# Optimization experiments

Hardware: AMD Instinct MI355X
Metric: run time of the kernel (lower is better)

## Reference

```python
import jax, jax.numpy as jnp
import numpy as np

N = 50000      # nodes per type
E = 600000     # edges per relation
D_IN = 128
D_OUT = 64


def setup_inputs() -> dict:
    key = jax.random.key(0)
    ks = jax.random.split(key, 12)
    x_v0 = jax.random.normal(ks[0], (N, D_IN), dtype=jnp.float32)
    x_v1 = jax.random.normal(ks[1], (N, D_IN), dtype=jnp.float32)
    edge_v0 = jax.random.randint(ks[2], (2, E), 0, N, dtype=jnp.int64)
    edge_v1 = jax.random.randint(ks[3], (2, E), 0, N, dtype=jnp.int64)
    s = 1.0 / np.sqrt(D_IN)
    Wrel0 = jax.random.uniform(ks[4], (D_OUT, D_IN), jnp.float32, -s, s)
    brel0 = jax.random.uniform(ks[5], (D_OUT,), jnp.float32, -s, s)
    Wroot0 = jax.random.uniform(ks[6], (D_OUT, D_IN), jnp.float32, -s, s)
    Wrel1 = jax.random.uniform(ks[7], (D_OUT, D_IN), jnp.float32, -s, s)
    brel1 = jax.random.uniform(ks[8], (D_OUT,), jnp.float32, -s, s)
    Wroot1 = jax.random.uniform(ks[9], (D_OUT, D_IN), jnp.float32, -s, s)
    sf = 1.0 / np.sqrt(2 * D_OUT)
    Wfc = jax.random.uniform(ks[10], (1, 2 * D_OUT), jnp.float32, -sf, sf)
    bfc = jax.random.uniform(ks[11], (1,), jnp.float32, -sf, sf)
    return {"x_v0": x_v0, "x_v1": x_v1, "edge_v0": edge_v0, "edge_v1": edge_v1,
            "Wrel0": Wrel0, "brel0": brel0, "Wroot0": Wroot0,
            "Wrel1": Wrel1, "brel1": brel1, "Wroot1": Wroot1,
            "Wfc": Wfc, "bfc": bfc}


def _graph_conv(x, edge_index, Wrel, brel, Wroot):
    # PyG GraphConv (aggr='add'): out = lin_rel(sum_{j in N(i)} x_j) + lin_root(x_i)
    src, dst = edge_index[0], edge_index[1]
    agg = jax.ops.segment_sum(x[src], dst, num_segments=x.shape[0])  # [N, D_IN]
    return agg @ Wrel.T + brel + x @ Wroot.T


def reference(x_v0, x_v1, edge_v0, edge_v1, Wrel0, brel0, Wroot0,
              Wrel1, brel1, Wroot1, Wfc, bfc):
    h0 = jax.nn.relu(_graph_conv(x_v0, edge_v0, Wrel0, brel0, Wroot0))  # [N, 64]
    h1 = jax.nn.relu(_graph_conv(x_v1, edge_v1, Wrel1, brel1, Wroot1))  # [N, 64]
    h = jnp.concatenate([h0, h1], axis=1)  # [N, 128]
    return h @ Wfc.T + bfc  # [N, 1]
```

## Files before the change

### kernel.cpp

```cpp
#include <hip/hip_runtime.h>
#include <hip/hip_bf16.h>

typedef __attribute__((ext_vector_type(8))) short short8;
typedef __attribute__((ext_vector_type(4))) float floatx4;

#define NB    1000
#define BPN   50
#define BCAP  832
#define CHUNK 2048

static __device__ __forceinline__ unsigned short bf16_of(float f) {
    union { float f; unsigned u; } v; v.f = f;
    unsigned r = (v.u + 0x7FFF + ((v.u >> 16) & 1)) >> 16;
    return (unsigned short)r;
}
static __device__ __forceinline__ float lo_f(unsigned u) {
    union { float f; unsigned u; } v; v.u = u << 16; return v.f;
}
static __device__ __forceinline__ float hi_f(unsigned u) {
    union { float f; unsigned u; } v; v.u = u & 0xFFFF0000u; return v.f;
}

__global__ __launch_bounds__(256) void convert_w(
    const float* __restrict__ Wrel0, const float* __restrict__ Wroot0,
    const float* __restrict__ Wrel1, const float* __restrict__ Wroot1,
    unsigned short* __restrict__ Wb0, unsigned short* __restrict__ Wb1)
{
    int c = blockIdx.x * 256 + threadIdx.x;
    if (c >= 4096) return;
    const float* s; unsigned short* d;
    if      (c < 1024) { s = Wrel0 + c * 8;           d = Wb0 + c * 8; }
    else if (c < 2048) { int t = c - 1024; s = Wroot0 + t * 8; d = Wb0 + 8192 + t * 8; }
    else if (c < 3072) { int t = c - 2048; s = Wrel1 + t * 8;  d = Wb1 + t * 8; }
    else               { int t = c - 3072; s = Wroot1 + t * 8; d = Wb1 + 8192 + t * 8; }

    floatx4 v0 = *(const floatx4*)s;
    floatx4 v1 = *(const floatx4*)(s + 4);
    short8 r = { (short)bf16_of(v0[0]), (short)bf16_of(v0[1]),
                 (short)bf16_of(v0[2]), (short)bf16_of(v0[3]),
                 (short)bf16_of(v1[0]), (short)bf16_of(v1[1]),
                 (short)bf16_of(v1[2]), (short)bf16_of(v1[3]) };
    *(short8*)d = r;
}

__global__ __launch_bounds__(256) void gemm_mfma(
    const float* __restrict__ X0, const float* __restrict__ X1,
    const unsigned short* __restrict__ Wb0, const unsigned short* __restrict__ Wb1,
    unsigned short* __restrict__ Yrel0, unsigned short* __restrict__ Yrel1,
    unsigned short* __restrict__ Yroot0, unsigned short* __restrict__ Yroot1,
    int N)
{
    const float* X           = blockIdx.y ? X1 : X0;
    const unsigned short* Wb = blockIdx.y ? Wb1 : Wb0;
    unsigned short* Yrel     = blockIdx.y ? Yrel1 : Yrel0;
    unsigned short* Yroot    = blockIdx.y ? Yroot1 : Yroot0;

    __shared__ __align__(16) short x_sh[128 * 136];
    __shared__ __align__(16) short w_sh[128 * 136];

    const int tid = threadIdx.x;
    const int m0  = blockIdx.x * 128;

#pragma unroll
    for (int i = 0; i < 8; ++i) {
        int c   = tid + 256 * i;
        int row = c >> 4;
        int kc  = (c & 15) * 8;
        *(short8*)&w_sh[row * 136 + kc] = *(const short8*)(Wb + row * 128 + kc);
    }
#pragma unroll
    for (int i = 0; i < 16; ++i) {
        int c    = tid + 256 * i;
        int row  = c >> 5;
        int f    = (c & 31) * 4;
        int node = m0 + row;
        floatx4 v = {};
        if (node < N) v = *(const floatx4*)(X + (size_t)node * 128 + f);
        short* d = &x_sh[row * 136 + f];
        d[0] = (short)bf16_of(v[0]); d[1] = (short)bf16_of(v[1]);
        d[2] = (short)bf16_of(v[2]); d[3] = (short)bf16_of(v[3]);
    }
    __syncthreads();

    const int wv   = tid >> 6;
    const int lane = tid & 63;
    const int q    = lane >> 4;
    const int r    = lane & 15;

    floatx4 acc[2][8] = {};
#pragma unroll
    for (int ko = 0; ko < 4; ++ko) {
        int kb = ko * 32 + q * 8;
        short8 a0 = *(const short8*)&x_sh[(wv * 32 + r) * 136 + kb];
        short8 a1 = *(const short8*)&x_sh[(wv * 32 + 16 + r) * 136 + kb];
#pragma unroll
        for (int nt = 0; nt < 8; ++nt) {
            short8 b = *(const short8*)&w_sh[(nt * 16 + r) * 136 + kb];
            acc[0][nt] = __builtin_amdgcn_mfma_f32_16x16x32_bf16(a0, b, acc[0][nt], 0, 0, 0);
            acc[1][nt] = __builtin_amdgcn_mfma_f32_16x16x32_bf16(a1, b, acc[1][nt], 0, 0, 0);
        }
    }

#pragma unroll
    for (int mt = 0; mt < 2; ++mt)
#pragma unroll
        for (int nt = 0; nt < 8; ++nt) {
            int col = nt * 16 + r;
#pragma unroll
            for (int reg = 0; reg < 4; ++reg) {
                int row = m0 + wv * 32 + mt * 16 + q * 4 + reg;
                if (row < N) {
                    if (nt < 4) Yrel[(size_t)row * 64 + col] = bf16_of(acc[mt][nt][reg]);
                    else        Yroot[(size_t)row * 64 + (col - 64)] = bf16_of(acc[mt][nt][reg]);
                }
            }
        }
}

__global__ __launch_bounds__(256) void bucket_pass(
    const int* __restrict__ e0, const int* __restrict__ e1,
    unsigned int* __restrict__ pairs0, unsigned int* __restrict__ pairs1,
    int* __restrict__ cur0, int* __restrict__ cur1, int E, int N)
{
    const int* e        = blockIdx.y ? e1 : e0;
    unsigned int* pairs = blockIdx.y ? pairs1 : pairs0;
    int* cur            = blockIdx.y ? cur1 : cur0;

    __shared__ unsigned int   stage[CHUNK];
    __shared__ unsigned short sbuck[CHUNK];
    __shared__ int hist[NB];
    __shared__ int loff[NB];
    __shared__ int lcur[NB];
    __shared__ int gbase[NB];
    __shared__ int scanb[256];

    const int tid = threadIdx.x;
    const int c0  = blockIdx.x * CHUNK;
    const int n   = min(CHUNK, E - c0);

    for (int b = tid; b < NB; b += 256) hist[b] = 0;
    __syncthreads();

#pragma unroll
    for (int k = 0; k < CHUNK / 256; ++k) {
        int i = c0 + k * 256 + tid;
        if (i < c0 + n) {
            int dst = e[E + i];
            if ((unsigned)dst < (unsigned)N)
                atomicAdd(&hist[(unsigned)dst / BPN], 1);
        }
    }
    __syncthreads();

    int t4 = tid * 4, v[4], s = 0;
#pragma unroll
    for (int k = 0; k < 4; ++k) {
        int b = t4 + k;
        v[k] = (b < NB) ? hist[b] : 0;
        s += v[k];
    }
    scanb[tid] = s;
    __syncthreads();
    for (int off = 1; off < 256; off <<= 1) {
        int x = (tid >= off) ? scanb[tid - off] : 0;
        __syncthreads();
        scanb[tid] += x;
        __syncthreads();
    }
    int run = scanb[tid] - s;
#pragma unroll
    for (int k = 0; k < 4; ++k) {
        int b = t4 + k;
        if (b < NB) { loff[b] = run; lcur[b] = run; }
        run += v[k];
    }
    for (int b = tid; b < NB; b += 256)
        gbase[b] = (hist[b] > 0) ? atomicAdd(&cur[b], hist[b]) : 0;
    __syncthreads();

#pragma unroll
    for (int k = 0; k < CHUNK / 256; ++k) {
        int i = c0 + k * 256 + tid;
        if (i < c0 + n) {
            int src = e[i];
            int dst = e[E + i];
            if ((unsigned)dst < (unsigned)N) {
                unsigned usrc = ((unsigned)src < (unsigned)N) ? (unsigned)src : 0u;
                int b = (unsigned)dst / BPN;
                int p = atomicAdd(&lcur[b], 1);
                stage[p] = ((unsigned)dst << 16) | usrc;
                sbuck[p] = (unsigned short)b;
            }
        }
    }
    __syncthreads();

    int total = scanb[255];
    for (int p = tid; p < total; p += 256) {
        int b = sbuck[p];
        int g = gbase[b] + (p - loff[b]);
        if (g < BCAP)
            pairs[(size_t)b * BCAP + g] = stage[p];
    }
}

__global__ __launch_bounds__(512) void bucket_gather(
    const unsigned int* __restrict__ pairs0, const unsigned int* __restrict__ pairs1,
    const int* __restrict__ cur0, const int* __restrict__ cur1,
    const unsigned short* __restrict__ Yrel0, const unsigned short* __restrict__ Yrel1,
    const unsigned short* __restrict__ Yroot0, const unsigned short* __restrict__ Yroot1,
    const float* __restrict__ brel0, const float* __restrict__ brel1,
    const float* __restrict__ wfc, const float* __restrict__ bfc,
    float* __restrict__ out, int N)
{
    __shared__ unsigned short slist0[BCAP], slist1[BCAP];
    __shared__ int cnt0s[BPN], cnt1s[BPN];
    __shared__ int off0s[BPN], off1s[BPN];
    __shared__ int cur0s[BPN], cur1s[BPN];

    const int tid  = threadIdx.x;
    const int b    = blockIdx.x;
    const int wv   = tid >> 6;
    const int lane = tid & 63;
    const int c    = lane & 31;
    const int half = lane >> 5;

    for (int i = tid; i < BPN; i += 512) { cnt0s[i] = 0; cnt1s[i] = 0; }
    __syncthreads();

    const int n0 = min(cur0[b], BCAP);
    const int n1 = min(cur1[b], BCAP);
    const unsigned base = (unsigned)(b * BPN);

    for (int j = tid; j < n0; j += 512)
        atomicAdd(&cnt0s[(pairs0[(size_t)b * BCAP + j] >> 16) - base], 1);
    for (int j = tid; j < n1; j += 512)
        atomicAdd(&cnt1s[(pairs1[(size_t)b * BCAP + j] >> 16) - base], 1);
    __syncthreads();

    if (wv == 0) {
        int cc = (lane < BPN) ? cnt0s[lane] : 0;
        int inc = cc;
#pragma unroll
        for (int d = 1; d < 64; d <<= 1) {
            int t = __shfl_up(inc, d, 64);
            if (lane >= d) inc += t;
        }
        if (lane < BPN) { off0s[lane] = inc - cc; cur0s[lane] = inc - cc; }
    } else if (wv == 1) {
        int cc = (lane < BPN) ? cnt1s[lane] : 0;
        int inc = cc;
#pragma unroll
        for (int d = 1; d < 64; d <<= 1) {
            int t = __shfl_up(inc, d, 64);
            if (lane >= d) inc += t;
        }
        if (lane < BPN) { off1s[lane] = inc - cc; cur1s[lane] = inc - cc; }
    }
    __syncthreads();

    for (int j = tid; j < n0; j += 512) {
        unsigned p = pairs0[(size_t)b * BCAP + j];
        int pos = atomicAdd(&cur0s[(p >> 16) - base], 1);
        slist0[pos] = (unsigned short)(p & 0xFFFFu);
    }
    for (int j = tid; j < n1; j += 512) {
        unsigned p = pairs1[(size_t)b * BCAP + j];
        int pos = atomicAdd(&cur1s[(p >> 16) - base], 1);
        slist1[pos] = (unsigned short)(p & 0xFFFFu);
    }
    __syncthreads();

    const float2 br0 = ((const float2*)brel0)[c];
    const float2 br1 = ((const float2*)brel1)[c];
    const float2 w0  = ((const float2*)wfc)[c];
    const float2 w1  = ((const float2*)(wfc + 64))[c];
    const float bias = bfc[0];

    for (int nl = wv; nl < BPN; nl += 8) {
        int i = b * BPN + nl;
        float a0x = 0.f, a0y = 0.f, a1x = 0.f, a1y = 0.f;

        {
            int st = off0s[nl], d = cnt0s[nl], j = 0;
            for (; j + 7 < d; j += 8) {
                int i0 = slist0[st + j + half];
                int i1 = slist0[st + j + 2 + half];
                int i2 = slist0[st + j + 4 + half];
                int i3 = slist0[st + j + 6 + half];
                unsigned u0 = ((const unsigned*)(Yrel0 + ((size_t)i0 << 6)))[c];
                unsigned u1 = ((const unsigned*)(Yrel0 + ((size_t)i1 << 6)))[c];
                unsigned u2 = ((const unsigned*)(Yrel0 + ((size_t)i2 << 6)))[c];
                unsigned u3 = ((const unsigned*)(Yrel0 + ((size_t)i3 << 6)))[c];
                a0x += (lo_f(u0) + lo_f(u1)) + (lo_f(u2) + lo_f(u3));
                a0y += (hi_f(u0) + hi_f(u1)) + (hi_f(u2) + hi_f(u3));
            }
            for (; j < d; j += 2) {
                int jj = j + half;
                int idx = slist0[st + (jj < d ? jj : d - 1)];
                unsigned u = ((const unsigned*)(Yrel0 + ((size_t)idx << 6)))[c];
                if (jj < d) { a0x += lo_f(u); a0y += hi_f(u); }
            }
        }
        {
            int st = off1s[nl], d = cnt1s[nl], j = 0;
            for (; j + 7 < d; j += 8) {
                int i0 = slist1[st + j + half];
                int i1 = slist1[st + j + 2 + half];
                int i2 = slist1[st + j + 4 + half];
                int i3 = slist1[st + j + 6 + half];
                unsigned u0 = ((const unsigned*)(Yrel1 + ((size_t)i0 << 6)))[c];
                unsigned u1 = ((const unsigned*)(Yrel1 + ((size_t)i1 << 6)))[c];
                unsigned u2 = ((const unsigned*)(Yrel1 + ((size_t)i2 << 6)))[c];
                unsigned u3 = ((const unsigned*)(Yrel1 + ((size_t)i3 << 6)))[c];
                a1x += (lo_f(u0) + lo_f(u1)) + (lo_f(u2) + lo_f(u3));
                a1y += (hi_f(u0) + hi_f(u1)) + (hi_f(u2) + hi_f(u3));
            }
            for (; j < d; j += 2) {
                int jj = j + half;
                int idx = slist1[st + (jj < d ? jj : d - 1)];
                unsigned u = ((const unsigned*)(Yrel1 + ((size_t)idx << 6)))[c];
                if (jj < d) { a1x += lo_f(u); a1y += hi_f(u); }
            }
        }

        a0x += __shfl_xor(a0x, 32, 64);
        a0y += __shfl_xor(a0y, 32, 64);
        a1x += __shfl_xor(a1x, 32, 64);
        a1y += __shfl_xor(a1y, 32, 64);

        unsigned ur0 = ((const unsigned*)(Yroot0 + ((size_t)i << 6)))[c];
        unsigned ur1 = ((const unsigned*)(Yroot1 + ((size_t)i << 6)))[c];

        float h0x = fmaxf(a0x + br0.x + lo_f(ur0), 0.f);
        float h0y = fmaxf(a0y + br0.y + hi_f(ur0), 0.f);
        float h1x = fmaxf(a1x + br1.x + lo_f(ur1), 0.f);
        float h1y = fmaxf(a1y + br1.y + hi_f(ur1), 0.f);
        float s = h0x * w0.x + h0y * w0.y + h1x * w1.x + h1y * w1.y;

#pragma unroll
        for (int m = 16; m > 0; m >>= 1) s += __shfl_xor(s, m, 64);
        if (lane == 0) out[i] = s + bias;
    }
}

extern "C" void kernel_launch(void* const* d_in, const int* in_sizes, int n_in,
                              void* d_out, int out_size, void* d_ws, size_t ws_size,
                              hipStream_t stream)
{
    const int N = in_sizes[0] / 128;
    const int E = in_sizes[2] / 2;

    const float* x0     = (const float*)d_in[0];
    const float* x1     = (const float*)d_in[1];
    const int*   e0     = (const int*)d_in[2];
    const int*   e1     = (const int*)d_in[3];
    const float* Wrel0  = (const float*)d_in[4];
    const float* brel0  = (const float*)d_in[5];
    const float* Wroot0 = (const float*)d_in[6];
    const float* Wrel1  = (const float*)d_in[7];
    const float* brel1  = (const float*)d_in[8];
    const float* Wroot1 = (const float*)d_in[9];
    const float* wfc    = (const float*)d_in[10];
    const float* bfc    = (const float*)d_in[11];
    float* out = (float*)d_out;

    unsigned short* Wb0   = (unsigned short*)d_ws;
    unsigned short* Wb1   = Wb0 + 128 * 128;
    unsigned short* Yrel0 = Wb1 + 128 * 128;
    unsigned short* Yrel1 = Yrel0 + (size_t)N * 64;
    unsigned short* Yroot0 = Yrel1 + (size_t)N * 64;
    unsigned short* Yroot1 = Yroot0 + (size_t)N * 64;
    unsigned int* pairs0 = (unsigned int*)(Yroot1 + (size_t)N * 64);
    unsigned int* pairs1 = pairs0 + (size_t)NB * BCAP;
    int* cur0 = (int*)(pairs1 + (size_t)NB * BCAP);
    int* cur1 = cur0 + NB;

    (void)hipMemsetAsync(cur0, 0, 2 * NB * sizeof(int), stream);

    convert_w<<<16, 256, 0, stream>>>(Wrel0, Wroot0, Wrel1, Wroot1, Wb0, Wb1);

    dim3 gemm_grid((N + 127) / 128, 2);
    gemm_mfma<<<gemm_grid, 256, 0, stream>>>(x0, x1, Wb0, Wb1,
                                             Yrel0, Yrel1, Yroot0, Yroot1, N);

    dim3 bp_grid((E + CHUNK - 1) / CHUNK, 2);
    bucket_pass<<<bp_grid, 256, 0, stream>>>(e0, e1, pairs0, pairs1,
                                             cur0, cur1, E, N);

    bucket_gather<<<NB, 512, 0, stream>>>(pairs0, pairs1, cur0, cur1,
                                          Yrel0, Yrel1, Yroot0, Yroot1,
                                          brel0, brel1, wfc, bfc, out, N);
}
```

Baseline: 193.1 us.

## Fuse GEMM and edge bucketing into one launch, fold memset into weight conversion

```diff
diff --git a/kernel.cpp b/kernel.cpp
--- a/kernel.cpp
+++ b/kernel.cpp
@@ -8,6 +8,7 @@
 #define BPN   50
 #define BCAP  832
 #define CHUNK 2048
+#define NPASS 293
 
 static __device__ __forceinline__ unsigned short bf16_of(float f) {
     union { float f; unsigned u; } v; v.f = f;
@@ -24,10 +25,14 @@
 __global__ __launch_bounds__(256) void convert_w(
     const float* __restrict__ Wrel0, const float* __restrict__ Wroot0,
     const float* __restrict__ Wrel1, const float* __restrict__ Wroot1,
-    unsigned short* __restrict__ Wb0, unsigned short* __restrict__ Wb1)
+    unsigned short* __restrict__ Wb0, unsigned short* __restrict__ Wb1,
+    int* __restrict__ cur0, int* __restrict__ cur1)
 {
     int c = blockIdx.x * 256 + threadIdx.x;
+    if (c < NB)          cur0[c] = 0;
+    else if (c < 2 * NB) cur1[c - NB] = 0;
     if (c >= 4096) return;
+
     const float* s; unsigned short* d;
     if      (c < 1024) { s = Wrel0 + c * 8;           d = Wb0 + c * 8; }
     else if (c < 2048) { int t = c - 1024; s = Wroot0 + t * 8; d = Wb0 + 8192 + t * 8; }
@@ -43,165 +48,163 @@
     *(short8*)d = r;
 }
 
-__global__ __launch_bounds__(256) void gemm_mfma(
+union SmemU {
+    struct { short x_sh[32 * 136]; short w_sh[128 * 136]; } g;
+    struct {
+        unsigned int   stage[CHUNK];
+        unsigned short sbuck[CHUNK];
+        int hist[NB]; int loff[NB]; int lcur[NB]; int gbase[NB];
+        int scanb[256];
+    } p;
+};
+
+__global__ __launch_bounds__(256) void gemm_and_pass(
     const float* __restrict__ X0, const float* __restrict__ X1,
     const unsigned short* __restrict__ Wb0, const unsigned short* __restrict__ Wb1,
     unsigned short* __restrict__ Yrel0, unsigned short* __restrict__ Yrel1,
     unsigned short* __restrict__ Yroot0, unsigned short* __restrict__ Yroot1,
-    int N)
+    const int* __restrict__ e0, const int* __restrict__ e1,
+    unsigned int* __restrict__ pairs0, unsigned int* __restrict__ pairs1,
+    int* __restrict__ cur0, int* __restrict__ cur1, int E, int N)
 {
-    const float* X           = blockIdx.y ? X1 : X0;
-    const unsigned short* Wb = blockIdx.y ? Wb1 : Wb0;
-    unsigned short* Yrel     = blockIdx.y ? Yrel1 : Yrel0;
-    unsigned short* Yroot    = blockIdx.y ? Yroot1 : Yroot0;
-
-    __shared__ __align__(16) short x_sh[128 * 136];
-    __shared__ __align__(16) short w_sh[128 * 136];
-
+    __shared__ __align__(16) SmemU sm;
     const int tid = threadIdx.x;
-    const int m0  = blockIdx.x * 128;
+    const int rel = blockIdx.y;
+
+    if (blockIdx.x < NPASS) {
+        const int* e        = rel ? e1 : e0;
+        unsigned int* pairs = rel ? pairs1 : pairs0;
+        int* cur            = rel ? cur1 : cur0;
+
+        const int c0 = blockIdx.x * CHUNK;
+        const int n  = min(CHUNK, E - c0);
+
+        for (int b = tid; b < NB; b += 256) sm.p.hist[b] = 0;
+        __syncthreads();
+
+        int dsts[CHUNK / 256];
+#pragma unroll
+        for (int k = 0; k < CHUNK / 256; ++k) {
+            int i = c0 + k * 256 + tid;
+            int dst = (i < c0 + n) ? e[E + i] : -1;
+            dsts[k] = dst;
+            if ((unsigned)dst < (unsigned)N)
+                atomicAdd(&sm.p.hist[(unsigned)dst / BPN], 1);
+        }
+        __syncthreads();
+
+        int t4 = tid * 4, v[4], s = 0;
+#pragma unroll
+        for (int k = 0; k < 4; ++k) {
+            int b = t4 + k;
+            v[k] = (b < NB) ? sm.p.hist[b] : 0;
+            s += v[k];
+        }
+        sm.p.scanb[tid] = s;
+        __syncthreads();
+        for (int off = 1; off < 256; off <<= 1) {
+            int x = (tid >= off) ? sm.p.scanb[tid - off] : 0;
+            __syncthreads();
+            sm.p.scanb[tid] += x;
+            __syncthreads();
+        }
+        int run = sm.p.scanb[tid] - s;
+#pragma unroll
+        for (int k = 0; k < 4; ++k) {
+            int b = t4 + k;
+            if (b < NB) { sm.p.loff[b] = run; sm.p.lcur[b] = run; }
+            run += v[k];
+        }
+        for (int b = tid; b < NB; b += 256)
+            sm.p.gbase[b] = (sm.p.hist[b] > 0) ? atomicAdd(&cur[b], sm.p.hist[b]) : 0;
+        __syncthreads();
+
+#pragma unroll
+        for (int k = 0; k < CHUNK / 256; ++k) {
+            int i   = c0 + k * 256 + tid;
+            int dst = dsts[k];
+            if ((unsigned)dst < (unsigned)N) {
+                int src = e[i];
+                unsigned usrc = ((unsigned)src < (unsigned)N) ? (unsigned)src : 0u;
+                int b = (unsigned)dst / BPN;
+                int p = atomicAdd(&sm.p.lcur[b], 1);
+                sm.p.stage[p] = ((unsigned)dst << 16) | usrc;
+                sm.p.sbuck[p] = (unsigned short)b;
+            }
+        }
+        __syncthreads();
+
+        int total = sm.p.scanb[255];
+        for (int p = tid; p < total; p += 256) {
+            int b = sm.p.sbuck[p];
+            int g = sm.p.gbase[b] + (p - sm.p.loff[b]);
+            if (g < BCAP)
+                pairs[(size_t)b * BCAP + g] = sm.p.stage[p];
+        }
+        return;
+    }
+
+    const float* X           = rel ? X1 : X0;
+    const unsigned short* Wb = rel ? Wb1 : Wb0;
+    unsigned short* Yrel     = rel ? Yrel1 : Yrel0;
+    unsigned short* Yroot    = rel ? Yroot1 : Yroot0;
+
+    const int m0 = (blockIdx.x - NPASS) * 32;
 
 #pragma unroll
     for (int i = 0; i < 8; ++i) {
         int c   = tid + 256 * i;
         int row = c >> 4;
         int kc  = (c & 15) * 8;
-        *(short8*)&w_sh[row * 136 + kc] = *(const short8*)(Wb + row * 128 + kc);
-    }
-#pragma unroll
-    for (int i = 0; i < 16; ++i) {
+        *(short8*)&sm.g.w_sh[row * 136 + kc] = *(const short8*)(Wb + row * 128 + kc);
+    }
+#pragma unroll
+    for (int i = 0; i < 4; ++i) {
         int c    = tid + 256 * i;
         int row  = c >> 5;
         int f    = (c & 31) * 4;
         int node = m0 + row;
         floatx4 v = {};
         if (node < N) v = *(const floatx4*)(X + (size_t)node * 128 + f);
-        short* d = &x_sh[row * 136 + f];
+        short* d = &sm.g.x_sh[row * 136 + f];
         d[0] = (short)bf16_of(v[0]); d[1] = (short)bf16_of(v[1]);
         d[2] = (short)bf16_of(v[2]); d[3] = (short)bf16_of(v[3]);
     }
     __syncthreads();
 
-    const int wv   = tid >> 6;
+    const int w    = tid >> 6;
     const int lane = tid & 63;
     const int q    = lane >> 4;
     const int r    = lane & 15;
 
-    floatx4 acc[2][8] = {};
+    floatx4 acc[2][2] = {};
 #pragma unroll
     for (int ko = 0; ko < 4; ++ko) {
         int kb = ko * 32 + q * 8;
-        short8 a0 = *(const short8*)&x_sh[(wv * 32 + r) * 136 + kb];
-        short8 a1 = *(const short8*)&x_sh[(wv * 32 + 16 + r) * 136 + kb];
-#pragma unroll
-        for (int nt = 0; nt < 8; ++nt) {
-            short8 b = *(const short8*)&w_sh[(nt * 16 + r) * 136 + kb];
-            acc[0][nt] = __builtin_amdgcn_mfma_f32_16x16x32_bf16(a0, b, acc[0][nt], 0, 0, 0);
-            acc[1][nt] = __builtin_amdgcn_mfma_f32_16x16x32_bf16(a1, b, acc[1][nt], 0, 0, 0);
-        }
+        short8 a0 = *(const short8*)&sm.g.x_sh[(r) * 136 + kb];
+        short8 a1 = *(const short8*)&sm.g.x_sh[(16 + r) * 136 + kb];
+        short8 b0 = *(const short8*)&sm.g.w_sh[(w * 32 + r) * 136 + kb];
+        short8 b1 = *(const short8*)&sm.g.w_sh[(w * 32 + 16 + r) * 136 + kb];
+        acc[0][0] = __builtin_amdgcn_mfma_f32_16x16x32_bf16(a0, b0, acc[0][0], 0, 0, 0);
+        acc[0][1] = __builtin_amdgcn_mfma_f32_16x16x32_bf16(a0, b1, acc[0][1], 0, 0, 0);
+        acc[1][0] = __builtin_amdgcn_mfma_f32_16x16x32_bf16(a1, b0, acc[1][0], 0, 0, 0);
+        acc[1][1] = __builtin_amdgcn_mfma_f32_16x16x32_bf16(a1, b1, acc[1][1], 0, 0, 0);
     }
 
 #pragma unroll
     for (int mt = 0; mt < 2; ++mt)
 #pragma unroll
-        for (int nt = 0; nt < 8; ++nt) {
-            int col = nt * 16 + r;
+        for (int nt = 0; nt < 2; ++nt) {
+            int col = w * 32 + nt * 16 + r;
 #pragma unroll
             for (int reg = 0; reg < 4; ++reg) {
-                int row = m0 + wv * 32 + mt * 16 + q * 4 + reg;
-                if (row < N) {
-                    if (nt < 4) Yrel[(size_t)row * 64 + col] = bf16_of(acc[mt][nt][reg]);
-                    else        Yroot[(size_t)row * 64 + (col - 64)] = bf16_of(acc[mt][nt][reg]);
+                int node = m0 + mt * 16 + q * 4 + reg;
+                if (node < N) {
+                    if (col < 64) Yrel[(size_t)node * 64 + col] = bf16_of(acc[mt][nt][reg]);
+                    else          Yroot[(size_t)node * 64 + (col - 64)] = bf16_of(acc[mt][nt][reg]);
                 }
             }
         }
-}
-
-__global__ __launch_bounds__(256) void bucket_pass(
-    const int* __restrict__ e0, const int* __restrict__ e1,
-    unsigned int* __restrict__ pairs0, unsigned int* __restrict__ pairs1,
-    int* __restrict__ cur0, int* __restrict__ cur1, int E, int N)
-{
-    const int* e        = blockIdx.y ? e1 : e0;
-    unsigned int* pairs = blockIdx.y ? pairs1 : pairs0;
-    int* cur            = blockIdx.y ? cur1 : cur0;
-
-    __shared__ unsigned int   stage[CHUNK];
-    __shared__ unsigned short sbuck[CHUNK];
-    __shared__ int hist[NB];
-    __shared__ int loff[NB];
-    __shared__ int lcur[NB];
-    __shared__ int gbase[NB];
-    __shared__ int scanb[256];
-
-    const int tid = threadIdx.x;
-    const int c0  = blockIdx.x * CHUNK;
-    const int n   = min(CHUNK, E - c0);
-
-    for (int b = tid; b < NB; b += 256) hist[b] = 0;
-    __syncthreads();
-
-#pragma unroll
-    for (int k = 0; k < CHUNK / 256; ++k) {
-        int i = c0 + k * 256 + tid;
-        if (i < c0 + n) {
-            int dst = e[E + i];
-            if ((unsigned)dst < (unsigned)N)
-                atomicAdd(&hist[(unsigned)dst / BPN], 1);
-        }
-    }
-    __syncthreads();
-
-    int t4 = tid * 4, v[4], s = 0;
-#pragma unroll
-    for (int k = 0; k < 4; ++k) {
-        int b = t4 + k;
-        v[k] = (b < NB) ? hist[b] : 0;
-        s += v[k];
-    }
-    scanb[tid] = s;
-    __syncthreads();
-    for (int off = 1; off < 256; off <<= 1) {
-        int x = (tid >= off) ? scanb[tid - off] : 0;
-        __syncthreads();
-        scanb[tid] += x;
-        __syncthreads();
-    }
-    int run = scanb[tid] - s;
-#pragma unroll
-    for (int k = 0; k < 4; ++k) {
-        int b = t4 + k;
-        if (b < NB) { loff[b] = run; lcur[b] = run; }
-        run += v[k];
-    }
-    for (int b = tid; b < NB; b += 256)
-        gbase[b] = (hist[b] > 0) ? atomicAdd(&cur[b], hist[b]) : 0;
-    __syncthreads();
-
-#pragma unroll
-    for (int k = 0; k < CHUNK / 256; ++k) {
-        int i = c0 + k * 256 + tid;
-        if (i < c0 + n) {
-            int src = e[i];
-            int dst = e[E + i];
-            if ((unsigned)dst < (unsigned)N) {
-                unsigned usrc = ((unsigned)src < (unsigned)N) ? (unsigned)src : 0u;
-                int b = (unsigned)dst / BPN;
-                int p = atomicAdd(&lcur[b], 1);
-                stage[p] = ((unsigned)dst << 16) | usrc;
-                sbuck[p] = (unsigned short)b;
-            }
-        }
-    }
-    __syncthreads();
-
-    int total = scanb[255];
-    for (int p = tid; p < total; p += 256) {
-        int b = sbuck[p];
-        int g = gbase[b] + (p - loff[b]);
-        if (g < BCAP)
-            pairs[(size_t)b * BCAP + g] = stage[p];
-    }
 }
 
 __global__ __launch_bounds__(512) void bucket_gather(
@@ -376,17 +379,14 @@
     int* cur0 = (int*)(pairs1 + (size_t)NB * BCAP);
     int* cur1 = cur0 + NB;
 
-    (void)hipMemsetAsync(cur0, 0, 2 * NB * sizeof(int), stream);
-
-    convert_w<<<16, 256, 0, stream>>>(Wrel0, Wroot0, Wrel1, Wroot1, Wb0, Wb1);
-
-    dim3 gemm_grid((N + 127) / 128, 2);
-    gemm_mfma<<<gemm_grid, 256, 0, stream>>>(x0, x1, Wb0, Wb1,
-                                             Yrel0, Yrel1, Yroot0, Yroot1, N);
-
-    dim3 bp_grid((E + CHUNK - 1) / CHUNK, 2);
-    bucket_pass<<<bp_grid, 256, 0, stream>>>(e0, e1, pairs0, pairs1,
-                                             cur0, cur1, E, N);
+    convert_w<<<16, 256, 0, stream>>>(Wrel0, Wroot0, Wrel1, Wroot1,
+                                      Wb0, Wb1, cur0, cur1);
+
+    const int gemm_nblk = (N + 31) / 32;
+    dim3 fused_grid(NPASS + gemm_nblk, 2);
+    gemm_and_pass<<<fused_grid, 256, 0, stream>>>(
+        x0, x1, Wb0, Wb1, Yrel0, Yrel1, Yroot0, Yroot1,
+        e0, e1, pairs0, pairs1, cur0, cur1, E, N);
 
     bucket_gather<<<NB, 512, 0, stream>>>(pairs0, pairs1, cur0, cur1,
                                           Yrel0, Yrel1, Yroot0, Yroot1,
```

Result: faster. 172.7 us (-10.6%).
